# Kernel optimization log

Hardware: AMD Instinct MI355X
Metric: run time of the kernel (lower is better)

## Reference

```python
import jax, jax.numpy as jnp
import numpy as np

TMP = 5.0  # temperature from init kwarg tmp=5

def _l2norm(x, axis, eps=1e-12):
    n = jnp.linalg.norm(x, axis=axis, keepdims=True)
    return x / jnp.maximum(n, eps)

def setup_inputs() -> dict:
    key = jax.random.key(0)
    ks = jax.random.split(key, 6)
    B, C, A, D, H = 128, 200, 312, 2048, 1600
    return {
        "AttM": jax.random.uniform(ks[0], (C, A), dtype=jnp.float32),
        "x_in": jax.random.uniform(ks[1], (B, D), dtype=jnp.float32),
        "Wg": jax.random.normal(ks[2], (A, D), dtype=jnp.float32) * 0.02,
        "bg": jnp.zeros((A,), jnp.float32),
        "W1": jax.random.normal(ks[3], (H, A), dtype=jnp.float32) * 0.02,
        "b1": jnp.zeros((H,), jnp.float32),
        "W2": jax.random.normal(ks[4], (D, H), dtype=jnp.float32) * 0.02,
        "b2": jnp.zeros((D,), jnp.float32),
        "bias_p": jnp.zeros((1,), jnp.float32),
        "scale_cls": jnp.full((1,), 10.0, jnp.float32),
    }

def reference(AttM, x_in, Wg, bg, W1, b1, W2, b2, bias_p, scale_cls):
    # x = F.normalize(input)  (p=2, dim=1)
    x = _l2norm(x_in, 1)                                   # [B, D]
    # attention over attribute dims from image features
    att = jax.nn.relu(x @ Wg.T + bg)                        # [B, A]
    att = jax.nn.softmax(att / TMP, axis=1)                 # [B, A]
    att = att[:, None, :] + 1.0                             # [B, 1, A] (att + ones)
    comb = att * AttM[None, :, :]                           # [B, C, A]
    # per-(sample,class) generated classifier via 2-layer MLP
    h = jax.nn.relu(jnp.einsum('bca,ha->bch', comb, W1) + b1)     # [B, C, 1600]
    cls = jax.nn.relu(jnp.einsum('bch,dh->bcd', h, W2) + b2)      # [B, C, D]
    cls = _l2norm(cls, -1)
    # original: matmul(classifier, x.T) -> [B,C,B], permute+diagonal -> [B,C].
    # Only the per-sample diagonal is kept, which equals a direct dot product:
    out = scale_cls[0] * (jnp.einsum('bcd,bd->bc', cls, x) + bias_p[0])  # [B, C]
    return out
```

## Files before the change

### kernel.cpp

```cpp
#include <hip/hip_runtime.h>
#include <hip/hip_bf16.h>
#include <math.h>

#define BB 128
#define CC 200
#define AA 312
#define AAP 320
#define DD 2048
#define HH 1600
#define HHP 1664
#define MM 25600

typedef __attribute__((ext_vector_type(8))) short bf16x8;
typedef __attribute__((ext_vector_type(4))) float f32x4;
typedef __attribute__((ext_vector_type(4))) unsigned short u16x4;

__device__ __forceinline__ unsigned short f2bf(float f) {
  union { float f; unsigned int u; } v; v.f = f;
  unsigned int u = v.u;
  unsigned int r = (u + 0x7fffu + ((u >> 16) & 1u)) >> 16;
  return (unsigned short)r;
}
__device__ __forceinline__ float bf2f(unsigned short b) {
  union { unsigned int u; float f; } v; v.u = ((unsigned int)b) << 16;
  return v.f;
}

__device__ __forceinline__ void gload_lds16(const void* g, void* l) {
  __builtin_amdgcn_global_load_lds(
      (const __attribute__((address_space(1))) unsigned int*)g,
      (__attribute__((address_space(3))) unsigned int*)l, 16, 0, 0);
}

__global__ __launch_bounds__(256)
void k_norm_attn(const float* __restrict__ x_in, const unsigned short* __restrict__ Wgb,
                 const float* __restrict__ bg, const float* __restrict__ AttM,
                 float* __restrict__ xf, unsigned short* __restrict__ comb) {
  int b = blockIdx.x;
  int t = threadIdx.x, wv = t >> 6, ln = t & 63;
  __shared__ float xs[DD];
  __shared__ float satt[AAP];
  __shared__ float wsum[4];
  if (t < AAP - AA) satt[AA + t] = 0.f;
  const float4* xi = (const float4*)(x_in + (size_t)b * DD);
  float4 v0 = xi[t], v1 = xi[t + 256];
  float s = v0.x*v0.x + v0.y*v0.y + v0.z*v0.z + v0.w*v0.w
          + v1.x*v1.x + v1.y*v1.y + v1.z*v1.z + v1.w*v1.w;
  for (int off = 32; off; off >>= 1) s += __shfl_xor(s, off, 64);
  if (ln == 0) wsum[wv] = s;
  __syncthreads();
  float sc = 1.f / fmaxf(sqrtf(wsum[0] + wsum[1] + wsum[2] + wsum[3]), 1e-12f);
  v0.x *= sc; v0.y *= sc; v0.z *= sc; v0.w *= sc;
  v1.x *= sc; v1.y *= sc; v1.z *= sc; v1.w *= sc;
  float4* xo = (float4*)(xf + (size_t)b * DD);
  xo[t] = v0; xo[t + 256] = v1;
  ((float4*)xs)[t] = v0; ((float4*)xs)[t + 256] = v1;
  __syncthreads();
  for (int a = wv; a < AA; a += 4) {
    const bf16x8* wrow = (const bf16x8*)(Wgb + (size_t)a * DD);
    float acc = 0.f;
#pragma unroll
    for (int j = 0; j < 4; j++) {
      bf16x8 w = wrow[j * 64 + ln];
      const float* xv = &xs[(j * 64 + ln) * 8];
#pragma unroll
      for (int e = 0; e < 8; e++) acc += bf2f((unsigned short)w[e]) * xv[e];
    }
    for (int off = 32; off; off >>= 1) acc += __shfl_xor(acc, off, 64);
    if (ln == 0) satt[a] = fmaxf(acc + bg[a], 0.f) * 0.2f;
  }
  __syncthreads();
  if (wv == 0) {
    float mx = -1e30f;
    for (int i = ln; i < AA; i += 64) mx = fmaxf(mx, satt[i]);
    for (int off = 32; off; off >>= 1) mx = fmaxf(mx, __shfl_xor(mx, off, 64));
    float ev[5]; float sm = 0.f;
#pragma unroll
    for (int k = 0; k < 5; k++) {
      int i = ln + k * 64;
      ev[k] = (i < AA) ? expf(satt[i] - mx) : 0.f;
      sm += ev[k];
    }
    for (int off = 32; off; off >>= 1) sm += __shfl_xor(sm, off, 64);
    float inv = 1.f / sm;
#pragma unroll
    for (int k = 0; k < 5; k++) {
      int i = ln + k * 64;
      if (i < AA) satt[i] = 1.f + ev[k] * inv;
    }
  }
  __syncthreads();
  const size_t mbase = (size_t)b * CC;
  for (int idx = t; idx < CC * 40; idx += 256) {
    int c = idx / 40, j = idx - c * 40;
    bf16x8 v = {};
    if (j < 39) {
      const float4* ap = (const float4*)(AttM + (size_t)c * AA + j * 8);
      float4 p0 = ap[0], p1 = ap[1];
      const float* sv = &satt[j * 8];
      v[0] = (short)f2bf(p0.x * sv[0]); v[1] = (short)f2bf(p0.y * sv[1]);
      v[2] = (short)f2bf(p0.z * sv[2]); v[3] = (short)f2bf(p0.w * sv[3]);
      v[4] = (short)f2bf(p1.x * sv[4]); v[5] = (short)f2bf(p1.y * sv[5]);
      v[6] = (short)f2bf(p1.z * sv[6]); v[7] = (short)f2bf(p1.w * sv[7]);
    }
    *(bf16x8*)(comb + (mbase + c) * AAP + j * 8) = v;
  }
}

#define R1SZ (HHP * AAP)
#define R2SZ (DD * HH)
#define R3SZ (AA * DD)
__global__ void k_cast_all(const float* __restrict__ W1, const float* __restrict__ W2,
                           const float* __restrict__ Wg, unsigned short* __restrict__ W1b,
                           unsigned short* __restrict__ W2b, unsigned short* __restrict__ Wgb) {
  int i = (blockIdx.x * 256 + threadIdx.x) * 4;
  if (i < R1SZ) {
    int r = i / AAP, c = i - r * AAP;
    u16x4 o = {};
    if (r < HH && c < AA) {
      float4 f = *(const float4*)(W1 + (size_t)r * AA + c);
      o[0] = f2bf(f.x); o[1] = f2bf(f.y); o[2] = f2bf(f.z); o[3] = f2bf(f.w);
    }
    *(u16x4*)(W1b + i) = o;
  } else if (i < R1SZ + R2SZ) {
    int j = i - R1SZ;
    float4 f = *(const float4*)(W2 + j);
    u16x4 o; o[0] = f2bf(f.x); o[1] = f2bf(f.y); o[2] = f2bf(f.z); o[3] = f2bf(f.w);
    *(u16x4*)(W2b + j) = o;
  } else if (i < R1SZ + R2SZ + R3SZ) {
    int j = i - R1SZ - R2SZ;
    float4 f = *(const float4*)(Wg + j);
    u16x4 o; o[0] = f2bf(f.x); o[1] = f2bf(f.y); o[2] = f2bf(f.z); o[3] = f2bf(f.w);
    *(u16x4*)(Wgb + j) = o;
  }
}

template <int KD, int NT>
__device__ __forceinline__ void gemm_core(const unsigned short* __restrict__ A,
                                          const unsigned short* __restrict__ Bm,
                                          short* As, short* Bs, f32x4 (&acc)[4][4],
                                          size_t ar0, size_t br0, int tid, int w, int ln) {
  const int scol = (((tid & 7) ^ ((tid >> 3) & 7)) << 3);
  const unsigned short* aP = A + (ar0 + (tid >> 3)) * KD + scol;
  const unsigned short* bP = Bm + (br0 + (tid >> 3)) * KD + scol;
  const int lr = ln & 15, hi = ln >> 4;
  const int axor0 = ((hi ^ (lr & 7)) << 3);
  const int axor1 = (((4 + hi) ^ (lr & 7)) << 3);
  const int wrow = (w >> 1) * 64, wcol = (w & 1) * 64;
  const int abase = (wrow + lr) * 64, bbase = (wcol + lr) * 64;
  for (int kt = 0; kt < NT; ++kt) {
#pragma unroll
    for (int p = 0; p < 4; p++) {
      gload_lds16(aP + (size_t)(p * 32) * KD + kt * 64, &As[p * 2048 + tid * 8]);
      gload_lds16(bP + (size_t)(p * 32) * KD + kt * 64, &Bs[p * 2048 + tid * 8]);
    }
    __syncthreads();
    bf16x8 av[4][2], bv[4][2];
#pragma unroll
    for (int i = 0; i < 4; i++) {
      av[i][0] = *(const bf16x8*)&As[abase + i * 1024 + axor0];
      av[i][1] = *(const bf16x8*)&As[abase + i * 1024 + axor1];
    }
#pragma unroll
    for (int i = 0; i < 4; i++) {
      bv[i][0] = *(const bf16x8*)&Bs[bbase + i * 1024 + axor0];
      bv[i][1] = *(const bf16x8*)&Bs[bbase + i * 1024 + axor1];
    }
#pragma unroll
    for (int m = 0; m < 4; m++)
#pragma unroll
      for (int n = 0; n < 4; n++) {
        acc[m][n] = __builtin_amdgcn_mfma_f32_16x16x32_bf16(av[m][0], bv[n][0], acc[m][n], 0, 0, 0);
        acc[m][n] = __builtin_amdgcn_mfma_f32_16x16x32_bf16(av[m][1], bv[n][1], acc[m][n], 0, 0, 0);
      }
    __syncthreads();
  }
}

__global__ __launch_bounds__(256, 4)
void k_gemm_h(const unsigned short* __restrict__ A, const unsigned short* __restrict__ Bm,
              const float* __restrict__ bias, unsigned short* __restrict__ C) {
  __shared__ short As[128 * 64];
  __shared__ short Bs[128 * 64];
  int tid = threadIdx.x, w = tid >> 6, ln = tid & 63;
  int bid = blockIdx.x + blockIdx.y * gridDim.x;
  int lid = (bid & 7) * 325 + (bid >> 3);
  int bx = lid % 13, by = lid / 13;
  f32x4 acc[4][4] = {};
  gemm_core<AAP, AAP / 64>(A, Bm, As, Bs, acc, (size_t)by * 128,
                           (size_t)bx * 128, tid, w, ln);
  int wrow = (w >> 1) * 64, wcol = (w & 1) * 64;
  int gr0 = by * 128 + wrow + (ln >> 4) * 4;
  int gc0 = bx * 128 + wcol + (ln & 15);
#pragma unroll
  for (int m = 0; m < 4; m++)
#pragma unroll
    for (int r = 0; r < 4; r++) {
      size_t grow = (size_t)(gr0 + m * 16 + r);
#pragma unroll
      for (int n = 0; n < 4; n++) {
        int gcol = gc0 + n * 16;
        if (gcol < HH) {
          float v = acc[m][n][r] + bias[gcol];
          C[grow * HH + gcol] = f2bf(fmaxf(v, 0.f));
        }
      }
    }
}

__global__ __launch_bounds__(256, 4)
void k_gemm_cls(const unsigned short* __restrict__ A, const unsigned short* __restrict__ Bm,
                const float* __restrict__ b2, const float* __restrict__ xf,
                float* __restrict__ dotb, float* __restrict__ nrm2b) {
  __shared__ short As[128 * 64];
  __shared__ short Bs[128 * 64];
  int tid = threadIdx.x, w = tid >> 6, ln = tid & 63;
  int bid = blockIdx.x + blockIdx.y * gridDim.x;
  int lid = (bid & 7) * 400 + (bid >> 3);
  int bx = lid & 15, by = lid >> 4;
  f32x4 acc[4][4] = {};
  gemm_core<HH, HH / 64>(A, Bm, As, Bs, acc, (size_t)by * 128,
                         (size_t)bx * 128, tid, w, ln);
  int wrow = (w >> 1) * 64, wcol = (w & 1) * 64;
  int gr0 = by * 128 + wrow + (ln >> 4) * 4;
  int gc0 = bx * 128 + wcol + (ln & 15);
  float bias[4];
#pragma unroll
  for (int n = 0; n < 4; n++) bias[n] = b2[gc0 + n * 16];
#pragma unroll
  for (int m = 0; m < 4; m++)
#pragma unroll
    for (int r = 0; r < 4; r++) {
      int grow = gr0 + m * 16 + r;
      int b = grow / CC;
      const float* xr = xf + (size_t)b * DD;
      float s1 = 0.f, s2 = 0.f;
#pragma unroll
      for (int n = 0; n < 4; n++) {
        float cls = fmaxf(acc[m][n][r] + bias[n], 0.f);
        s1 += cls * cls;
        s2 += cls * xr[gc0 + n * 16];
      }
      s1 += __shfl_xor(s1, 1, 64); s2 += __shfl_xor(s2, 1, 64);
      s1 += __shfl_xor(s1, 2, 64); s2 += __shfl_xor(s2, 2, 64);
      s1 += __shfl_xor(s1, 4, 64); s2 += __shfl_xor(s2, 4, 64);
      s1 += __shfl_xor(s1, 8, 64); s2 += __shfl_xor(s2, 8, 64);
      if ((ln & 15) == 0) {
        atomicAdd(&nrm2b[grow], s1);
        atomicAdd(&dotb[grow], s2);
      }
    }
}

__global__ void k_final(const float* __restrict__ dotb, const float* __restrict__ nrm2b,
                        const float* __restrict__ bias_p, const float* __restrict__ scale_cls,
                        float* __restrict__ out) {
  int i = blockIdx.x * 256 + threadIdx.x;
  if (i < MM)
    out[i] = scale_cls[0] * (dotb[i] / fmaxf(sqrtf(nrm2b[i]), 1e-12f) + bias_p[0]);
}

extern "C" void kernel_launch(void* const* d_in, const int* in_sizes, int n_in,
                              void* d_out, int out_size, void* d_ws, size_t ws_size,
                              hipStream_t stream) {
  const float* AttM = (const float*)d_in[0];
  const float* x_in = (const float*)d_in[1];
  const float* Wg = (const float*)d_in[2];
  const float* bg = (const float*)d_in[3];
  const float* W1 = (const float*)d_in[4];
  const float* b1 = (const float*)d_in[5];
  const float* W2 = (const float*)d_in[6];
  const float* b2 = (const float*)d_in[7];
  const float* bias_p = (const float*)d_in[8];
  const float* scale_cls = (const float*)d_in[9];
  float* out = (float*)d_out;

  char* ws = (char*)d_ws;
  size_t off = 0;
  auto alloc = [&](size_t bytes) {
    char* p = ws + off;
    off += (bytes + 255) & ~(size_t)255;
    return p;
  };
  float* xf = (float*)alloc((size_t)BB * DD * 4);
  unsigned short* comb = (unsigned short*)alloc((size_t)MM * AAP * 2);
  unsigned short* W1b = (unsigned short*)alloc((size_t)R1SZ * 2);
  unsigned short* W2b = (unsigned short*)alloc((size_t)R2SZ * 2);
  unsigned short* Wgb = (unsigned short*)alloc((size_t)R3SZ * 2);
  unsigned short* hbuf = (unsigned short*)alloc((size_t)MM * HH * 2);
  float* dotb = (float*)alloc((size_t)MM * 4);
  float* nrm2b = (float*)alloc((size_t)MM * 4);
  (void)ws_size; (void)in_sizes; (void)n_in; (void)out_size;

  hipMemsetAsync(dotb, 0, (size_t)MM * 4 * 2, stream);

  k_cast_all<<<((R1SZ + R2SZ + R3SZ) / 4 + 255) / 256, 256, 0, stream>>>(W1, W2, Wg, W1b, W2b, Wgb);
  k_norm_attn<<<BB, 256, 0, stream>>>(x_in, Wgb, bg, AttM, xf, comb);
  k_gemm_h<<<dim3(13, MM / 128), 256, 0, stream>>>(comb, W1b, b1, hbuf);
  k_gemm_cls<<<dim3(DD / 128, MM / 128), 256, 0, stream>>>(hbuf, W2b, b2, xf, dotb, nrm2b);
  k_final<<<(MM + 255) / 256, 256, 0, stream>>>(dotb, nrm2b, bias_p, scale_cls, out);
}
```

Baseline: 315.4 us.

## Use 256x256 tiles with 8 waves and double-buffered LDS in classifier GEMM

Replaces the 128x128, 4-wave classifier GEMM with a 256x256 tile kernel using 512 threads, where each wave holds a 128x64 accumulator block. K tiles are double-buffered with direct global-to-LDS loads, explicit vmcnt waits, XOR-swizzled LDS reads and setprio around the MFMA groups. The aim is more operand reuse per byte loaded and overlap of loads with MFMA. In exchange it uses more LDS and registers and runs fewer blocks, only 800 CTAs.

```diff
diff --git a/kernel.cpp b/kernel.cpp
--- a/kernel.cpp
+++ b/kernel.cpp
@@ -10,6 +10,7 @@
 #define HH 1600
 #define HHP 1664
 #define MM 25600
+#define NKTC 25
 
 typedef __attribute__((ext_vector_type(8))) short bf16x8;
 typedef __attribute__((ext_vector_type(4))) float f32x4;
@@ -208,30 +209,115 @@
     }
 }
 
-__global__ __launch_bounds__(256, 4)
-void k_gemm_cls(const unsigned short* __restrict__ A, const unsigned short* __restrict__ Bm,
-                const float* __restrict__ b2, const float* __restrict__ xf,
-                float* __restrict__ dotb, float* __restrict__ nrm2b) {
-  __shared__ short As[128 * 64];
-  __shared__ short Bs[128 * 64];
-  int tid = threadIdx.x, w = tid >> 6, ln = tid & 63;
-  int bid = blockIdx.x + blockIdx.y * gridDim.x;
-  int lid = (bid & 7) * 400 + (bid >> 3);
-  int bx = lid & 15, by = lid >> 4;
-  f32x4 acc[4][4] = {};
-  gemm_core<HH, HH / 64>(A, Bm, As, Bs, acc, (size_t)by * 128,
-                         (size_t)bx * 128, tid, w, ln);
-  int wrow = (w >> 1) * 64, wcol = (w & 1) * 64;
-  int gr0 = by * 128 + wrow + (ln >> 4) * 4;
-  int gc0 = bx * 128 + wcol + (ln & 15);
+
+#define BARRIER asm volatile("s_barrier" ::: "memory")
+
+#define ISSUE_A(buf, kt, h)                                                        \
+  do {                                                                             \
+    gload_lds16(aRow + (size_t)((h) * 128) * HH + (size_t)(kt) * 64,               \
+                &LA[buf][(h) * 8192 + ldsw]);                                      \
+    gload_lds16(aRow + (size_t)((h) * 128 + 64) * HH + (size_t)(kt) * 64,          \
+                &LA[buf][(h) * 8192 + 4096 + ldsw]);                               \
+  } while (0)
+#define ISSUE_B(buf, kt, h)                                                        \
+  do {                                                                             \
+    gload_lds16(bRow + (size_t)((h) * 128) * HH + (size_t)(kt) * 64,               \
+                &LB[buf][(h) * 8192 + ldsw]);                                      \
+    gload_lds16(bRow + (size_t)((h) * 128 + 64) * HH + (size_t)(kt) * 64,          \
+                &LB[buf][(h) * 8192 + 4096 + ldsw]);                               \
+  } while (0)
+
+#define READ_A(mh)                                                                 \
+  do {                                                                             \
+    _Pragma("unroll") for (int m = 0; m < 4; m++) {                                \
+      int rr = abase + ((mh) * 4 + m) * 1024;                                      \
+      av[m][0] = *(const bf16x8*)&LA[cur][rr + axor0];                             \
+      av[m][1] = *(const bf16x8*)&LA[cur][rr + axor1];                             \
+    }                                                                              \
+  } while (0)
+#define READ_B(nh)                                                                 \
+  do {                                                                             \
+    _Pragma("unroll") for (int n = 0; n < 2; n++) {                                \
+      int rr = bbase + ((nh) * 2 + n) * 1024;                                      \
+      bv[(nh) * 2 + n][0] = *(const bf16x8*)&LB[cur][rr + axor0];                  \
+      bv[(nh) * 2 + n][1] = *(const bf16x8*)&LB[cur][rr + axor1];                  \
+    }                                                                              \
+  } while (0)
+
+#define MFMA1(d, a_, b_) d = __builtin_amdgcn_mfma_f32_16x16x32_bf16(a_, b_, d, 0, 0, 0)
+#define MFMA_Q(MB, NB)                                                             \
+  do {                                                                             \
+    __builtin_amdgcn_s_setprio(1);                                                 \
+    _Pragma("unroll") for (int mm = 0; mm < 4; mm++)                               \
+    _Pragma("unroll") for (int nn = 0; nn < 2; nn++) {                             \
+      MFMA1(acc[(MB) + mm][(NB) + nn], av[mm][0], bv[(NB) + nn][0]);               \
+      MFMA1(acc[(MB) + mm][(NB) + nn], av[mm][1], bv[(NB) + nn][1]);               \
+    }                                                                              \
+    __builtin_amdgcn_s_setprio(0);                                                 \
+  } while (0)
+
+__global__ __launch_bounds__(512, 2)
+void k_gemm_cls8(const unsigned short* __restrict__ A,
+                 const unsigned short* __restrict__ Bm,
+                 const float* __restrict__ b2, const float* __restrict__ xf,
+                 float* __restrict__ dotb, float* __restrict__ nrm2b) {
+  __shared__ short LA[2][16384];
+  __shared__ short LB[2][16384];
+  const int tid = threadIdx.x, w = tid >> 6, ln = tid & 63;
+  const int wr = w >> 2, wc = w & 3;
+  const int lr = ln & 15, hi = ln >> 4;
+  const int bid = (int)(blockIdx.x + blockIdx.y * gridDim.x);
+  const int lid = (bid & 7) * 100 + (bid >> 3);
+  const size_t m0 = (size_t)(lid >> 3) * 256;
+  const size_t n0 = (size_t)(lid & 7) * 256;
+  const int scol = (((tid & 7) ^ ((tid >> 3) & 7)) << 3);
+  const unsigned short* aRow = A + (m0 + (tid >> 3)) * HH + scol;
+  const unsigned short* bRow = Bm + (n0 + (tid >> 3)) * HH + scol;
+  const int ldsw = w * 512;
+
+  const int axor0 = ((hi ^ (lr & 7)) << 3);
+  const int axor1 = (((4 + hi) ^ (lr & 7)) << 3);
+  const int abase = (wr * 128 + lr) * 64;
+  const int bbase = (wc * 64 + lr) * 64;
+
+  f32x4 acc[8][4] = {};
+  bf16x8 av[4][2], bv[4][2];
+
+  ISSUE_A(0, 0, 0); ISSUE_A(0, 0, 1);
+  ISSUE_B(0, 0, 0); ISSUE_B(0, 0, 1);
+
+  int cur = 0;
+  for (int kt = 0; kt < NKTC; ++kt) {
+    const int nxt = cur ^ 1;
+    if (kt < NKTC - 1) {
+      ISSUE_A(nxt, kt + 1, 0); ISSUE_A(nxt, kt + 1, 1);
+      ISSUE_B(nxt, kt + 1, 0); ISSUE_B(nxt, kt + 1, 1);
+      asm volatile("s_waitcnt vmcnt(8)" ::: "memory");
+    } else {
+      asm volatile("s_waitcnt vmcnt(0)" ::: "memory");
+    }
+    BARRIER;
+    READ_A(0); READ_B(0);
+    MFMA_Q(0, 0);
+    READ_B(1);
+    MFMA_Q(0, 2);
+    READ_A(1);
+    MFMA_Q(4, 2);
+    MFMA_Q(4, 0);
+    BARRIER;
+    cur = nxt;
+  }
+
+  const int gc0 = (int)n0 + wc * 64 + lr;
   float bias[4];
 #pragma unroll
   for (int n = 0; n < 4; n++) bias[n] = b2[gc0 + n * 16];
-#pragma unroll
-  for (int m = 0; m < 4; m++)
+  const int grow_base = (int)m0 + wr * 128 + hi * 4;
+#pragma unroll
+  for (int m = 0; m < 8; m++) {
 #pragma unroll
     for (int r = 0; r < 4; r++) {
-      int grow = gr0 + m * 16 + r;
+      int grow = grow_base + m * 16 + r;
       int b = grow / CC;
       const float* xr = xf + (size_t)b * DD;
       float s1 = 0.f, s2 = 0.f;
@@ -245,11 +331,12 @@
       s1 += __shfl_xor(s1, 2, 64); s2 += __shfl_xor(s2, 2, 64);
       s1 += __shfl_xor(s1, 4, 64); s2 += __shfl_xor(s2, 4, 64);
       s1 += __shfl_xor(s1, 8, 64); s2 += __shfl_xor(s2, 8, 64);
-      if ((ln & 15) == 0) {
+      if (lr == 0) {
         atomicAdd(&nrm2b[grow], s1);
         atomicAdd(&dotb[grow], s2);
       }
     }
+  }
 }
 
 __global__ void k_final(const float* __restrict__ dotb, const float* __restrict__ nrm2b,
@@ -297,6 +384,6 @@
   k_cast_all<<<((R1SZ + R2SZ + R3SZ) / 4 + 255) / 256, 256, 0, stream>>>(W1, W2, Wg, W1b, W2b, Wgb);
   k_norm_attn<<<BB, 256, 0, stream>>>(x_in, Wgb, bg, AttM, xf, comb);
   k_gemm_h<<<dim3(13, MM / 128), 256, 0, stream>>>(comb, W1b, b1, hbuf);
-  k_gemm_cls<<<dim3(DD / 128, MM / 128), 256, 0, stream>>>(hbuf, W2b, b2, xf, dotb, nrm2b);
+  k_gemm_cls8<<<dim3(DD / 256, MM / 256), 512, 0, stream>>>(hbuf, W2b, b2, xf, dotb, nrm2b);
   k_final<<<(MM + 255) / 256, 256, 0, stream>>>(dotb, nrm2b, bias_p, scale_cls, out);
 }
```

Result: slower. 393.3 us (+24.7%).

## Run second MLP GEMM in FP8 e4m3 with scaled MFMA

Applied to the files above, without the earlier changes.

Stores the hidden activations and W2 as FP8 e4m3 with fixed power-of-two prescales, padded to K=1664. The big second GEMM now uses the 16x16x128 f8f6f4 scaled MFMA with 128-byte K tiles. The accumulator is rescaled in the epilogue. This halves the bytes for the hidden buffer and W2 and doubles the matrix throughput per instruction, at the cost of extra quantization error in the classifier.

```diff
diff --git a/kernel.cpp b/kernel.cpp
--- a/kernel.cpp
+++ b/kernel.cpp
@@ -1,5 +1,6 @@
 #include <hip/hip_runtime.h>
 #include <hip/hip_bf16.h>
+#include <hip/hip_fp8.h>
 #include <math.h>
 
 #define BB 128
@@ -10,10 +11,16 @@
 #define HH 1600
 #define HHP 1664
 #define MM 25600
+#define KB8 1664
+#define NKT8 13
+#define SH 8.0f
+#define SW 32.0f
 
 typedef __attribute__((ext_vector_type(8))) short bf16x8;
 typedef __attribute__((ext_vector_type(4))) float f32x4;
 typedef __attribute__((ext_vector_type(4))) unsigned short u16x4;
+typedef __attribute__((ext_vector_type(8))) int i32x8;
+typedef __attribute__((ext_vector_type(4))) int i32x4;
 
 __device__ __forceinline__ unsigned short f2bf(float f) {
   union { float f; unsigned int u; } v; v.f = f;
@@ -24,6 +31,10 @@
 __device__ __forceinline__ float bf2f(unsigned short b) {
   union { unsigned int u; float f; } v; v.u = ((unsigned int)b) << 16;
   return v.f;
+}
+__device__ __forceinline__ unsigned char f2fp8(float f) {
+  __hip_fp8_e4m3 t(f);
+  return (unsigned char)t.__x;
 }
 
 __device__ __forceinline__ void gload_lds16(const void* g, void* l) {
@@ -108,11 +119,11 @@
 }
 
 #define R1SZ (HHP * AAP)
-#define R2SZ (DD * HH)
+#define R2SZ8 (DD * KB8)
 #define R3SZ (AA * DD)
 __global__ void k_cast_all(const float* __restrict__ W1, const float* __restrict__ W2,
                            const float* __restrict__ Wg, unsigned short* __restrict__ W1b,
-                           unsigned short* __restrict__ W2b, unsigned short* __restrict__ Wgb) {
+                           unsigned char* __restrict__ W2b8, unsigned short* __restrict__ Wgb) {
   int i = (blockIdx.x * 256 + threadIdx.x) * 4;
   if (i < R1SZ) {
     int r = i / AAP, c = i - r * AAP;
@@ -122,13 +133,18 @@
       o[0] = f2bf(f.x); o[1] = f2bf(f.y); o[2] = f2bf(f.z); o[3] = f2bf(f.w);
     }
     *(u16x4*)(W1b + i) = o;
-  } else if (i < R1SZ + R2SZ) {
+  } else if (i < R1SZ + R2SZ8) {
     int j = i - R1SZ;
-    float4 f = *(const float4*)(W2 + j);
-    u16x4 o; o[0] = f2bf(f.x); o[1] = f2bf(f.y); o[2] = f2bf(f.z); o[3] = f2bf(f.w);
-    *(u16x4*)(W2b + j) = o;
-  } else if (i < R1SZ + R2SZ + R3SZ) {
-    int j = i - R1SZ - R2SZ;
+    int r = j / KB8, c = j - r * KB8;
+    uchar4 o = make_uchar4(0, 0, 0, 0);
+    if (c < HH) {
+      float4 f = *(const float4*)(W2 + (size_t)r * HH + c);
+      o.x = f2fp8(f.x * SW); o.y = f2fp8(f.y * SW);
+      o.z = f2fp8(f.z * SW); o.w = f2fp8(f.w * SW);
+    }
+    *(uchar4*)(W2b8 + j) = o;
+  } else if (i < R1SZ + R2SZ8 + R3SZ) {
+    int j = i - R1SZ - R2SZ8;
     float4 f = *(const float4*)(Wg + j);
     u16x4 o; o[0] = f2bf(f.x); o[1] = f2bf(f.y); o[2] = f2bf(f.z); o[3] = f2bf(f.w);
     *(u16x4*)(Wgb + j) = o;
@@ -179,7 +195,7 @@
 
 __global__ __launch_bounds__(256, 4)
 void k_gemm_h(const unsigned short* __restrict__ A, const unsigned short* __restrict__ Bm,
-              const float* __restrict__ bias, unsigned short* __restrict__ C) {
+              const float* __restrict__ bias, unsigned char* __restrict__ C8) {
   __shared__ short As[128 * 64];
   __shared__ short Bs[128 * 64];
   int tid = threadIdx.x, w = tid >> 6, ln = tid & 63;
@@ -200,30 +216,69 @@
 #pragma unroll
       for (int n = 0; n < 4; n++) {
         int gcol = gc0 + n * 16;
-        if (gcol < HH) {
-          float v = acc[m][n][r] + bias[gcol];
-          C[grow * HH + gcol] = f2bf(fmaxf(v, 0.f));
-        }
+        float v = (gcol < HH) ? fmaxf(acc[m][n][r] + bias[gcol], 0.f) * SH : 0.f;
+        C8[grow * KB8 + gcol] = f2fp8(v);
       }
     }
 }
 
 __global__ __launch_bounds__(256, 4)
-void k_gemm_cls(const unsigned short* __restrict__ A, const unsigned short* __restrict__ Bm,
-                const float* __restrict__ b2, const float* __restrict__ xf,
-                float* __restrict__ dotb, float* __restrict__ nrm2b) {
-  __shared__ short As[128 * 64];
-  __shared__ short Bs[128 * 64];
+void k_gemm_cls_f8(const unsigned char* __restrict__ A,
+                   const unsigned char* __restrict__ Bm,
+                   const float* __restrict__ b2, const float* __restrict__ xf,
+                   float* __restrict__ dotb, float* __restrict__ nrm2b) {
+  __shared__ unsigned char As[128 * 128];
+  __shared__ unsigned char Bs[128 * 128];
   int tid = threadIdx.x, w = tid >> 6, ln = tid & 63;
   int bid = blockIdx.x + blockIdx.y * gridDim.x;
   int lid = (bid & 7) * 400 + (bid >> 3);
   int bx = lid & 15, by = lid >> 4;
+  size_t ar0 = (size_t)by * 128, br0 = (size_t)bx * 128;
+  const int scol = (((tid & 7) ^ ((tid >> 3) & 7)) << 4);
+  const unsigned char* aP = A + (ar0 + (tid >> 3)) * KB8 + scol;
+  const unsigned char* bP = Bm + (br0 + (tid >> 3)) * KB8 + scol;
+  const int lr = ln & 15, hi = ln >> 4;
+  const int s0 = hi * 2;
+  const int axor0 = ((s0 ^ (lr & 7)) << 4);
+  const int axor1 = (((s0 + 1) ^ (lr & 7)) << 4);
+  const int wrow = (w >> 1) * 64, wcol = (w & 1) * 64;
+  const int abase = (wrow + lr) * 128, bbase = (wcol + lr) * 128;
   f32x4 acc[4][4] = {};
-  gemm_core<HH, HH / 64>(A, Bm, As, Bs, acc, (size_t)by * 128,
-                         (size_t)bx * 128, tid, w, ln);
-  int wrow = (w >> 1) * 64, wcol = (w & 1) * 64;
-  int gr0 = by * 128 + wrow + (ln >> 4) * 4;
-  int gc0 = bx * 128 + wcol + (ln & 15);
+  for (int kt = 0; kt < NKT8; ++kt) {
+#pragma unroll
+    for (int p = 0; p < 4; p++) {
+      gload_lds16(aP + (size_t)(p * 32) * KB8 + kt * 128, &As[p * 4096 + tid * 16]);
+      gload_lds16(bP + (size_t)(p * 32) * KB8 + kt * 128, &Bs[p * 4096 + tid * 16]);
+    }
+    __syncthreads();
+    i32x8 av[4], bv[4];
+#pragma unroll
+    for (int i = 0; i < 4; i++) {
+      i32x4 q0 = *(const i32x4*)&As[abase + i * 2048 + axor0];
+      i32x4 q1 = *(const i32x4*)&As[abase + i * 2048 + axor1];
+      i32x8 t; t[0]=q0[0]; t[1]=q0[1]; t[2]=q0[2]; t[3]=q0[3];
+      t[4]=q1[0]; t[5]=q1[1]; t[6]=q1[2]; t[7]=q1[3];
+      av[i] = t;
+    }
+#pragma unroll
+    for (int i = 0; i < 4; i++) {
+      i32x4 q0 = *(const i32x4*)&Bs[bbase + i * 2048 + axor0];
+      i32x4 q1 = *(const i32x4*)&Bs[bbase + i * 2048 + axor1];
+      i32x8 t; t[0]=q0[0]; t[1]=q0[1]; t[2]=q0[2]; t[3]=q0[3];
+      t[4]=q1[0]; t[5]=q1[1]; t[6]=q1[2]; t[7]=q1[3];
+      bv[i] = t;
+    }
+#pragma unroll
+    for (int m = 0; m < 4; m++)
+#pragma unroll
+      for (int n = 0; n < 4; n++)
+        acc[m][n] = __builtin_amdgcn_mfma_scale_f32_16x16x128_f8f6f4(
+            av[m], bv[n], acc[m][n], 0, 0, 0, 127, 0, 127);
+    __syncthreads();
+  }
+  const float inv = 1.f / (SH * SW);
+  int gr0 = by * 128 + wrow + hi * 4;
+  int gc0 = bx * 128 + wcol + lr;
   float bias[4];
 #pragma unroll
   for (int n = 0; n < 4; n++) bias[n] = b2[gc0 + n * 16];
@@ -237,7 +292,7 @@
       float s1 = 0.f, s2 = 0.f;
 #pragma unroll
       for (int n = 0; n < 4; n++) {
-        float cls = fmaxf(acc[m][n][r] + bias[n], 0.f);
+        float cls = fmaxf(acc[m][n][r] * inv + bias[n], 0.f);
         s1 += cls * cls;
         s2 += cls * xr[gc0 + n * 16];
       }
@@ -245,7 +300,7 @@
       s1 += __shfl_xor(s1, 2, 64); s2 += __shfl_xor(s2, 2, 64);
       s1 += __shfl_xor(s1, 4, 64); s2 += __shfl_xor(s2, 4, 64);
       s1 += __shfl_xor(s1, 8, 64); s2 += __shfl_xor(s2, 8, 64);
-      if ((ln & 15) == 0) {
+      if (lr == 0) {
         atomicAdd(&nrm2b[grow], s1);
         atomicAdd(&dotb[grow], s2);
       }
@@ -285,18 +340,18 @@
   float* xf = (float*)alloc((size_t)BB * DD * 4);
   unsigned short* comb = (unsigned short*)alloc((size_t)MM * AAP * 2);
   unsigned short* W1b = (unsigned short*)alloc((size_t)R1SZ * 2);
-  unsigned short* W2b = (unsigned short*)alloc((size_t)R2SZ * 2);
+  unsigned char* W2b8 = (unsigned char*)alloc((size_t)R2SZ8);
   unsigned short* Wgb = (unsigned short*)alloc((size_t)R3SZ * 2);
-  unsigned short* hbuf = (unsigned short*)alloc((size_t)MM * HH * 2);
+  unsigned char* hbuf8 = (unsigned char*)alloc((size_t)MM * KB8);
   float* dotb = (float*)alloc((size_t)MM * 4);
   float* nrm2b = (float*)alloc((size_t)MM * 4);
   (void)ws_size; (void)in_sizes; (void)n_in; (void)out_size;
 
   hipMemsetAsync(dotb, 0, (size_t)MM * 4 * 2, stream);
 
-  k_cast_all<<<((R1SZ + R2SZ + R3SZ) / 4 + 255) / 256, 256, 0, stream>>>(W1, W2, Wg, W1b, W2b, Wgb);
+  k_cast_all<<<((R1SZ + R2SZ8 + R3SZ) / 4 + 255) / 256, 256, 0, stream>>>(W1, W2, Wg, W1b, W2b8, Wgb);
   k_norm_attn<<<BB, 256, 0, stream>>>(x_in, Wgb, bg, AttM, xf, comb);
-  k_gemm_h<<<dim3(13, MM / 128), 256, 0, stream>>>(comb, W1b, b1, hbuf);
-  k_gemm_cls<<<dim3(DD / 128, MM / 128), 256, 0, stream>>>(hbuf, W2b, b2, xf, dotb, nrm2b);
+  k_gemm_h<<<dim3(13, MM / 128), 256, 0, stream>>>(comb, W1b, b1, hbuf8);
+  k_gemm_cls_f8<<<dim3(DD / 128, MM / 128), 256, 0, stream>>>(hbuf8, W2b8, b2, xf, dotb, nrm2b);
   k_final<<<(MM + 255) / 256, 256, 0, stream>>>(dotb, nrm2b, bias_p, scale_cls, out);
 }
```

Result: slower. 1.104 ms (+249.9%).
